# Kernel optimization log

Hardware: AMD Instinct MI355X
Metric: run time of the kernel (lower is better)

## Reference

```python
import jax, jax.numpy as jnp
import numpy as np

EPS = 1e-7

def _dubbed_squash(v):
    norm = jnp.linalg.norm(v, axis=-1, keepdims=True)
    coef = 1.0 - 1.0 / (jnp.exp(norm) + EPS)
    return coef * v / (norm + EPS)

def setup_inputs() -> dict:
    key = jax.random.key(0)
    k1, k2, k3 = jax.random.split(key, 3)
    B, N, dp = 16, 1152, 8   # batch, num_primary_caps, dim_primary_caps
    D, dd = 10, 16           # num_digit_caps, dim_digit_caps
    primary_caps = jax.random.normal(k1, (B, N, dp), dtype=jnp.float32)
    W = jax.random.normal(k2, (D, N, dd, dp), dtype=jnp.float32) * 0.05
    B_prior = jax.random.normal(k3, (D, 1, N), dtype=jnp.float32) * 0.05
    return {"primary_caps": primary_caps, "W": W, "B_prior": B_prior}

def reference(primary_caps, W, B_prior):
    dp = primary_caps.shape[-1]
    # votes: U_hat[b,d,n,j] = W[d,n,j,i] @ u[b,n,i]   (replaces the tf.map_fn)
    U_hat = jnp.einsum('dnji,bni->bdnj', W, primary_caps)  # [B,D,N,dd]
    # self-similarity score matrix (as in original: full NxN matmul)
    A = jnp.einsum('bdnj,bdmj->bdnm', U_hat, U_hat) / jnp.sqrt(
        jnp.asarray(dp, dtype=primary_caps.dtype))          # [B,D,N,N]
    A_sum = jnp.sum(A, axis=2, keepdims=True)               # [B,D,1,N]
    C = jax.nn.softmax(A_sum, axis=1)                       # softmax over digit axis
    # weighted combine with learned log-priors: (B+C) @ U_hat -> [B,D,1,dd] -> squeeze
    S = jnp.einsum('bdkn,bdnj->bdj', B_prior[None] + C, U_hat)  # [B,D,dd]
    return _dubbed_squash(S)
```

## Files before the change

### kernel.cpp

```cpp
#include <hip/hip_runtime.h>
#include <hip/hip_bf16.h>

constexpr int BN = 16, NN = 1152, DP = 8, ND = 10, DD = 16;
constexpr int NCHA = 4;
constexpr int NCHB = 2;

__device__ __forceinline__ void load8(const float* __restrict__ p, float* dst) {
    const float4 a = reinterpret_cast<const float4*>(p)[0];
    const float4 b = reinterpret_cast<const float4*>(p)[1];
    dst[0] = a.x; dst[1] = a.y; dst[2] = a.z; dst[3] = a.w;
    dst[4] = b.x; dst[5] = b.y; dst[6] = b.z; dst[7] = b.w;
}

__global__ __launch_bounds__(256) void caps_T(
    const float* __restrict__ u, const float* __restrict__ W,
    float* __restrict__ T)
{
    const int j = threadIdx.x & 15, b = threadIdx.x >> 4;
    const int n0 = blockIdx.x * NCHA;
    float Tacc[ND];
#pragma unroll
    for (int d = 0; d < ND; ++d) Tacc[d] = 0.f;

    for (int nn = 0; nn < NCHA; ++nn) {
        const int n = n0 + nn;
        float uf[DP];
        load8(u + ((size_t)b * NN + n) * DP, uf);
#pragma unroll
        for (int d = 0; d < ND; ++d) {
            float wf[DP];
            load8(W + (((size_t)d * NN + n) * DD + j) * DP, wf);
            float s = 0.f;
#pragma unroll
            for (int i = 0; i < DP; ++i) s += wf[i] * uf[i];
            Tacc[d] += s;
        }
    }
#pragma unroll
    for (int d = 0; d < ND; ++d)
        atomicAdd(&T[((size_t)b * ND + d) * DD + j], Tacc[d]);
}

__global__ __launch_bounds__(256) void caps_S(
    const float* __restrict__ u, const float* __restrict__ W,
    const float* __restrict__ Bp, const float* __restrict__ T,
    float* __restrict__ S)
{
    const int j = threadIdx.x & 15, b = threadIdx.x >> 4;
    constexpr float RS8 = 0.35355339059327373f;

    float Treg[ND];
#pragma unroll
    for (int q = 0; q < ND; ++q) Treg[q] = T[((size_t)b * ND + q) * DD + j];

    float Sacc[ND];
#pragma unroll
    for (int q = 0; q < ND; ++q) Sacc[q] = 0.f;

    const int n0 = blockIdx.x * NCHB;
    for (int nn = 0; nn < NCHB; ++nn) {
        const int n = n0 + nn;
        float uf[DP];
        load8(u + ((size_t)b * NN + n) * DP, uf);

        float uh[ND], a[ND];
#pragma unroll
        for (int q = 0; q < ND; ++q) {
            float wf[DP];
            load8(W + (((size_t)q * NN + n) * DD + j) * DP, wf);
            float s = 0.f;
#pragma unroll
            for (int i = 0; i < DP; ++i) s += wf[i] * uf[i];
            uh[q] = s;
            float v = Treg[q] * s;
            v += __shfl_xor(v, 8, 16);
            v += __shfl_xor(v, 4, 16);
            v += __shfl_xor(v, 2, 16);
            v += __shfl_xor(v, 1, 16);
            a[q] = v * RS8;
        }
        float m = a[0];
#pragma unroll
        for (int q = 1; q < ND; ++q) m = fmaxf(m, a[q]);
        float e[ND], se = 0.f;
#pragma unroll
        for (int q = 0; q < ND; ++q) { e[q] = expf(a[q] - m); se += e[q]; }
        const float inv_se = 1.f / se;
#pragma unroll
        for (int q = 0; q < ND; ++q)
            Sacc[q] += (Bp[q * NN + n] + e[q] * inv_se) * uh[q];
    }
#pragma unroll
    for (int q = 0; q < ND; ++q)
        atomicAdd(&S[((size_t)b * ND + q) * DD + j], Sacc[q]);
}

__global__ __launch_bounds__(256) void caps_out(
    const float* __restrict__ S, float* __restrict__ out)
{
    const int idx = blockIdx.x * 256 + threadIdx.x;
    const float Sv = S[idx];
    float n2 = Sv * Sv;
#pragma unroll
    for (int off = 8; off >= 1; off >>= 1) n2 += __shfl_xor(n2, off, 16);
    const float nrm = sqrtf(n2);
    const float coef = 1.f - 1.f / (expf(nrm) + 1e-7f);
    out[idx] = Sv * (coef / (nrm + 1e-7f));
}

extern "C" void kernel_launch(void* const* d_in, const int* in_sizes, int n_in,
                              void* d_out, int out_size, void* d_ws, size_t ws_size,
                              hipStream_t stream) {
    const float* u  = nullptr;
    const float* W  = nullptr;
    const float* Bp = nullptr;
    for (int i = 0; i < n_in; ++i) {
        const int s = in_sizes[i];
        if (s == BN * NN * DP)            u  = (const float*)d_in[i];
        else if (s == ND * NN * DD * DP)  W  = (const float*)d_in[i];
        else if (s == ND * NN)            Bp = (const float*)d_in[i];
    }
    float* out = (float*)d_out;
    float* T = (float*)d_ws;
    float* S = T + BN * ND * DD;

    hipMemsetAsync(d_ws, 0, 2 * BN * ND * DD * sizeof(float), stream);
    caps_T  <<<dim3(NN / NCHA), 256, 0, stream>>>(u, W, T);
    caps_S  <<<dim3(NN / NCHB), 256, 0, stream>>>(u, W, Bp, T, S);
    caps_out<<<dim3(BN * ND * DD / 256), 256, 0, stream>>>(S, out);
}
```

Baseline: 94.08 us.

## Replace global atomics with per-block partials and dedicated reduction kernels

Each block of the T and S stages now writes its partial sums to its own slice of workspace instead of atomically adding into a shared accumulator. Separate reduction kernels sum the partials, and the final one is fused with the squash epilogue, which also removes the memset. This targets heavy atomic contention on a small number of addresses. In exchange it adds an extra launch, several MB of workspace traffic, and reduction kernels with only ten blocks and long serial loops.

```diff
diff --git a/kernel.cpp b/kernel.cpp
--- a/kernel.cpp
+++ b/kernel.cpp
@@ -3,7 +3,10 @@
 
 constexpr int BN = 16, NN = 1152, DP = 8, ND = 10, DD = 16;
 constexpr int NCHA = 4;
+constexpr int NBLK_A = NN / NCHA;
 constexpr int NCHB = 2;
+constexpr int NBLK_B = NN / NCHB;
+constexpr int CELLS = BN * ND * DD;
 
 __device__ __forceinline__ void load8(const float* __restrict__ p, float* dst) {
     const float4 a = reinterpret_cast<const float4*>(p)[0];
@@ -14,9 +17,9 @@
 
 __global__ __launch_bounds__(256) void caps_T(
     const float* __restrict__ u, const float* __restrict__ W,
-    float* __restrict__ T)
+    float* __restrict__ Tp)
 {
-    const int j = threadIdx.x & 15, b = threadIdx.x >> 4;
+    const int t = threadIdx.x, j = t & 15, b = t >> 4;
     const int n0 = blockIdx.x * NCHA;
     float Tacc[ND];
 #pragma unroll
@@ -36,22 +39,36 @@
             Tacc[d] += s;
         }
     }
+    float* dst = Tp + (size_t)blockIdx.x * CELLS;
 #pragma unroll
-    for (int d = 0; d < ND; ++d)
-        atomicAdd(&T[((size_t)b * ND + d) * DD + j], Tacc[d]);
+    for (int d = 0; d < ND; ++d) dst[d * 256 + t] = Tacc[d];
+}
+
+__global__ __launch_bounds__(256) void reduce_T(
+    const float* __restrict__ Tp, float* __restrict__ T)
+{
+    const int cell = blockIdx.x * 256 + threadIdx.x;
+    float s0 = 0.f, s1 = 0.f, s2 = 0.f, s3 = 0.f;
+    for (int c = 0; c < NBLK_A; c += 4) {
+        s0 += Tp[(size_t)(c + 0) * CELLS + cell];
+        s1 += Tp[(size_t)(c + 1) * CELLS + cell];
+        s2 += Tp[(size_t)(c + 2) * CELLS + cell];
+        s3 += Tp[(size_t)(c + 3) * CELLS + cell];
+    }
+    T[cell] = (s0 + s1) + (s2 + s3);
 }
 
 __global__ __launch_bounds__(256) void caps_S(
     const float* __restrict__ u, const float* __restrict__ W,
     const float* __restrict__ Bp, const float* __restrict__ T,
-    float* __restrict__ S)
+    float* __restrict__ Sp)
 {
-    const int j = threadIdx.x & 15, b = threadIdx.x >> 4;
+    const int t = threadIdx.x, j = t & 15, b = t >> 4;
     constexpr float RS8 = 0.35355339059327373f;
 
     float Treg[ND];
 #pragma unroll
-    for (int q = 0; q < ND; ++q) Treg[q] = T[((size_t)b * ND + q) * DD + j];
+    for (int q = 0; q < ND; ++q) Treg[q] = T[q * 256 + t];
 
     float Sacc[ND];
 #pragma unroll
@@ -90,22 +107,31 @@
         for (int q = 0; q < ND; ++q)
             Sacc[q] += (Bp[q * NN + n] + e[q] * inv_se) * uh[q];
     }
+    float* dst = Sp + (size_t)blockIdx.x * CELLS;
 #pragma unroll
-    for (int q = 0; q < ND; ++q)
-        atomicAdd(&S[((size_t)b * ND + q) * DD + j], Sacc[q]);
+    for (int q = 0; q < ND; ++q) dst[q * 256 + t] = Sacc[q];
 }
 
-__global__ __launch_bounds__(256) void caps_out(
-    const float* __restrict__ S, float* __restrict__ out)
+__global__ __launch_bounds__(256) void reduce_S_out(
+    const float* __restrict__ Sp, float* __restrict__ out)
 {
-    const int idx = blockIdx.x * 256 + threadIdx.x;
-    const float Sv = S[idx];
+    const int q = blockIdx.x, t = threadIdx.x;
+    const int cell = q * 256 + t;
+    float s0 = 0.f, s1 = 0.f, s2 = 0.f, s3 = 0.f;
+    for (int c = 0; c < NBLK_B; c += 4) {
+        s0 += Sp[(size_t)(c + 0) * CELLS + cell];
+        s1 += Sp[(size_t)(c + 1) * CELLS + cell];
+        s2 += Sp[(size_t)(c + 2) * CELLS + cell];
+        s3 += Sp[(size_t)(c + 3) * CELLS + cell];
+    }
+    const float Sv = (s0 + s1) + (s2 + s3);
     float n2 = Sv * Sv;
 #pragma unroll
     for (int off = 8; off >= 1; off >>= 1) n2 += __shfl_xor(n2, off, 16);
     const float nrm = sqrtf(n2);
     const float coef = 1.f - 1.f / (expf(nrm) + 1e-7f);
-    out[idx] = Sv * (coef / (nrm + 1e-7f));
+    const int b = t >> 4, j = t & 15;
+    out[((size_t)b * ND + q) * DD + j] = Sv * (coef / (nrm + 1e-7f));
 }
 
 extern "C" void kernel_launch(void* const* d_in, const int* in_sizes, int n_in,
@@ -121,11 +147,12 @@
         else if (s == ND * NN)            Bp = (const float*)d_in[i];
     }
     float* out = (float*)d_out;
-    float* T = (float*)d_ws;
-    float* S = T + BN * ND * DD;
+    float* Tp = (float*)d_ws;
+    float* T  = Tp + (size_t)NBLK_A * CELLS;
+    float* Sp = T + CELLS;
 
-    hipMemsetAsync(d_ws, 0, 2 * BN * ND * DD * sizeof(float), stream);
-    caps_T  <<<dim3(NN / NCHA), 256, 0, stream>>>(u, W, T);
-    caps_S  <<<dim3(NN / NCHB), 256, 0, stream>>>(u, W, Bp, T, S);
-    caps_out<<<dim3(BN * ND * DD / 256), 256, 0, stream>>>(S, out);
+    caps_T      <<<dim3(NBLK_A), 256, 0, stream>>>(u, W, Tp);
+    reduce_T    <<<dim3(CELLS / 256), 256, 0, stream>>>(Tp, T);
+    caps_S      <<<dim3(NBLK_B), 256, 0, stream>>>(u, W, Bp, T, Sp);
+    reduce_S_out<<<dim3(ND), 256, 0, stream>>>(Sp, out);
 }
```

Result: slower. 146.0 us (+55.2%).

## Split atomic accumulators four ways and fuse squash into last block

Applied to the files above, without the earlier changes.

Accumulates T and S into four separate copies chosen by block index, so fewer blocks contend on the same atomic addresses. The squash kernel is removed: a global ticket counter lets the last caps_S block sum the partial copies and write the output. caps_T now uses chunks of 2 instead of 4, which doubles its grid size. The cost is one kernel launch saved and less atomic contention, against more atomics from caps_T and a serial tail in the final block.

```diff
diff --git a/kernel.cpp b/kernel.cpp
--- a/kernel.cpp
+++ b/kernel.cpp
@@ -2,8 +2,10 @@
 #include <hip/hip_bf16.h>
 
 constexpr int BN = 16, NN = 1152, DP = 8, ND = 10, DD = 16;
-constexpr int NCHA = 4;
-constexpr int NCHB = 2;
+constexpr int NCH = 2;
+constexpr int NBLK = NN / NCH;
+constexpr int CELLS = BN * ND * DD;
+constexpr int SPLIT = 4;
 
 __device__ __forceinline__ void load8(const float* __restrict__ p, float* dst) {
     const float4 a = reinterpret_cast<const float4*>(p)[0];
@@ -14,15 +16,15 @@
 
 __global__ __launch_bounds__(256) void caps_T(
     const float* __restrict__ u, const float* __restrict__ W,
-    float* __restrict__ T)
+    float* __restrict__ Tsp)
 {
-    const int j = threadIdx.x & 15, b = threadIdx.x >> 4;
-    const int n0 = blockIdx.x * NCHA;
+    const int t = threadIdx.x, j = t & 15, b = t >> 4;
+    const int n0 = blockIdx.x * NCH;
     float Tacc[ND];
 #pragma unroll
     for (int d = 0; d < ND; ++d) Tacc[d] = 0.f;
 
-    for (int nn = 0; nn < NCHA; ++nn) {
+    for (int nn = 0; nn < NCH; ++nn) {
         const int n = n0 + nn;
         float uf[DP];
         load8(u + ((size_t)b * NN + n) * DP, uf);
@@ -36,33 +38,40 @@
             Tacc[d] += s;
         }
     }
+    float* Tdst = Tsp + (size_t)(blockIdx.x & (SPLIT - 1)) * CELLS;
 #pragma unroll
     for (int d = 0; d < ND; ++d)
-        atomicAdd(&T[((size_t)b * ND + d) * DD + j], Tacc[d]);
+        atomicAdd(&Tdst[d * 256 + t], Tacc[d]);
 }
 
 __global__ __launch_bounds__(256) void caps_S(
     const float* __restrict__ u, const float* __restrict__ W,
-    const float* __restrict__ Bp, const float* __restrict__ T,
-    float* __restrict__ S)
+    const float* __restrict__ Bp, const float* __restrict__ Tsp,
+    float* __restrict__ Ssp, unsigned* __restrict__ counter,
+    float* __restrict__ out)
 {
-    const int j = threadIdx.x & 15, b = threadIdx.x >> 4;
+    __shared__ unsigned ticket_s;
+    const int t = threadIdx.x, j = t & 15, b = t >> 4;
     constexpr float RS8 = 0.35355339059327373f;
 
     float Treg[ND];
 #pragma unroll
-    for (int q = 0; q < ND; ++q) Treg[q] = T[((size_t)b * ND + q) * DD + j];
+    for (int q = 0; q < ND; ++q) {
+        float s = 0.f;
+#pragma unroll
+        for (int p = 0; p < SPLIT; ++p) s += Tsp[(size_t)p * CELLS + q * 256 + t];
+        Treg[q] = s;
+    }
 
     float Sacc[ND];
 #pragma unroll
     for (int q = 0; q < ND; ++q) Sacc[q] = 0.f;
 
-    const int n0 = blockIdx.x * NCHB;
-    for (int nn = 0; nn < NCHB; ++nn) {
+    const int n0 = blockIdx.x * NCH;
+    for (int nn = 0; nn < NCH; ++nn) {
         const int n = n0 + nn;
         float uf[DP];
         load8(u + ((size_t)b * NN + n) * DP, uf);
-
         float uh[ND], a[ND];
 #pragma unroll
         for (int q = 0; q < ND; ++q) {
@@ -90,22 +99,31 @@
         for (int q = 0; q < ND; ++q)
             Sacc[q] += (Bp[q * NN + n] + e[q] * inv_se) * uh[q];
     }
+    float* Sdst = Ssp + (size_t)(blockIdx.x & (SPLIT - 1)) * CELLS;
 #pragma unroll
     for (int q = 0; q < ND; ++q)
-        atomicAdd(&S[((size_t)b * ND + q) * DD + j], Sacc[q]);
-}
+        atomicAdd(&Sdst[q * 256 + t], Sacc[q]);
 
-__global__ __launch_bounds__(256) void caps_out(
-    const float* __restrict__ S, float* __restrict__ out)
-{
-    const int idx = blockIdx.x * 256 + threadIdx.x;
-    const float Sv = S[idx];
-    float n2 = Sv * Sv;
+    __threadfence();
+    if (t == 0) ticket_s = atomicAdd(counter, 1u);
+    __syncthreads();
+    if (ticket_s == NBLK - 1) {
+        __threadfence();
 #pragma unroll
-    for (int off = 8; off >= 1; off >>= 1) n2 += __shfl_xor(n2, off, 16);
-    const float nrm = sqrtf(n2);
-    const float coef = 1.f - 1.f / (expf(nrm) + 1e-7f);
-    out[idx] = Sv * (coef / (nrm + 1e-7f));
+        for (int d = 0; d < ND; ++d) {
+            float Sv = 0.f;
+#pragma unroll
+            for (int p = 0; p < SPLIT; ++p)
+                Sv += atomicAdd(&Ssp[(size_t)p * CELLS + d * 256 + t], 0.f);
+            float n2 = Sv * Sv;
+#pragma unroll
+            for (int off = 8; off >= 1; off >>= 1)
+                n2 += __shfl_xor(n2, off, 16);
+            const float nrm = sqrtf(n2);
+            const float coef = 1.f - 1.f / (expf(nrm) + 1e-7f);
+            out[((size_t)b * ND + d) * DD + j] = Sv * (coef / (nrm + 1e-7f));
+        }
+    }
 }
 
 extern "C" void kernel_launch(void* const* d_in, const int* in_sizes, int n_in,
@@ -121,11 +139,13 @@
         else if (s == ND * NN)            Bp = (const float*)d_in[i];
     }
     float* out = (float*)d_out;
-    float* T = (float*)d_ws;
-    float* S = T + BN * ND * DD;
+    float* Tsp = (float*)d_ws;
+    float* Ssp = Tsp + (size_t)SPLIT * CELLS;
+    unsigned* counter = (unsigned*)(Ssp + (size_t)SPLIT * CELLS);
 
-    hipMemsetAsync(d_ws, 0, 2 * BN * ND * DD * sizeof(float), stream);
-    caps_T  <<<dim3(NN / NCHA), 256, 0, stream>>>(u, W, T);
-    caps_S  <<<dim3(NN / NCHB), 256, 0, stream>>>(u, W, Bp, T, S);
-    caps_out<<<dim3(BN * ND * DD / 256), 256, 0, stream>>>(S, out);
+    hipMemsetAsync(d_ws, 0,
+                   (2 * SPLIT * CELLS) * sizeof(float) + sizeof(unsigned),
+                   stream);
+    caps_T<<<dim3(NBLK), 256, 0, stream>>>(u, W, Tsp);
+    caps_S<<<dim3(NBLK), 256, 0, stream>>>(u, W, Bp, Tsp, Ssp, counter, out);
 }
```

Measured after the change: 121.9 us. +29.6%, slower.
